# Optimization experiments

Hardware: AMD Instinct MI355X
Metric: run time of the kernel (lower is better)

## Reference

```python
import jax, jax.numpy as jnp
import numpy as np
from jax import lax

B, S, F, H, V, T = 64, 1024, 128, 512, 64, 64
SOS, EOS = 0, 1


def lstm_cell(x, h, c, W_ih, W_hh, b_ih, b_hh):
    # PyTorch LSTM gate order: i, f, g, o
    gates = x @ W_ih.T + h @ W_hh.T + b_ih + b_hh  # [B, 4H]
    i, f, g, o = jnp.split(gates, 4, axis=-1)
    c_new = jax.nn.sigmoid(f) * c + jax.nn.sigmoid(i) * jnp.tanh(g)
    h_new = jax.nn.sigmoid(o) * jnp.tanh(c_new)
    return h_new, c_new


def setup_inputs() -> dict:
    key = jax.random.key(0)
    ks = jax.random.split(key, 12)
    s = 0.05  # weight scale to avoid gate saturation
    return {
        "signal": jax.random.normal(ks[0], (B, S, F), jnp.float32),
        "target": jax.random.randint(ks[1], (B, T), 0, V),
        "enc_W_ih": jax.random.normal(ks[2], (4 * H, F), jnp.float32) * s,
        "enc_W_hh": jax.random.normal(ks[3], (4 * H, H), jnp.float32) * s,
        "enc_b_ih": jax.random.normal(ks[4], (4 * H,), jnp.float32) * s,
        "enc_b_hh": jax.random.normal(ks[5], (4 * H,), jnp.float32) * s,
        "dec_W_ih": jax.random.normal(ks[6], (4 * H, V), jnp.float32) * s,
        "dec_W_hh": jax.random.normal(ks[7], (4 * H, H), jnp.float32) * s,
        "dec_b_ih": jax.random.normal(ks[8], (4 * H,), jnp.float32) * s,
        "dec_b_hh": jax.random.normal(ks[9], (4 * H,), jnp.float32) * s,
        "out_W": jax.random.normal(ks[10], (V, H), jnp.float32) * s,
        "out_b": jax.random.normal(ks[11], (V,), jnp.float32) * s,
    }


def reference(signal, target, enc_W_ih, enc_W_hh, enc_b_ih, enc_b_hh,
              dec_W_ih, dec_W_hh, dec_b_ih, dec_b_hh, out_W, out_b):
    b = signal.shape[0]
    hdim = enc_W_hh.shape[1]
    vocab = out_b.shape[0]
    n_steps = target.shape[1]  # max_loop = target.size(1)

    # ---- encoder LSTM (only final hidden state is used downstream) ----
    def enc_step(carry, x_t):
        h, c = carry
        h, c = lstm_cell(x_t, h, c, enc_W_ih, enc_W_hh, enc_b_ih, enc_b_hh)
        return (h, c), None

    h0 = jnp.zeros((b, hdim), signal.dtype)
    (h, c), _ = lax.scan(enc_step, (h0, h0), jnp.swapaxes(signal, 0, 1))

    # ---- decoder: teacher-start (one-hot target[:,0]) then greedy feedback ----
    inp0 = jax.nn.one_hot(target[:, 0], vocab, dtype=signal.dtype)  # [B, V]

    def dec_step(carry, _):
        h, c, x = carry
        x = jax.nn.relu(x)  # F.relu on one-hot input (faithful to source)
        h, c = lstm_cell(x, h, c, dec_W_ih, dec_W_hh, dec_b_ih, dec_b_hh)
        logits = h @ out_W.T + out_b  # [B, V]
        nxt = jax.nn.one_hot(jnp.argmax(logits, axis=-1), vocab, dtype=x.dtype)
        return (h, c, nxt), logits

    (_, _, _), logits = lax.scan(dec_step, (h, c, inp0), None, length=n_steps)
    logits = jnp.swapaxes(logits, 0, 1)  # [B, T, V]
    return jax.nn.log_softmax(logits, axis=-1)
```

## Files before the change

kernel.cpp:

```cpp
#include <hip/hip_runtime.h>
#include <cstddef>
#include <math.h>

#define NGROUP 4
#define WPG    32
#define NWG    128
#define BPG    16
#define BB  64
#define HH  512
#define TT  64
#define VV  64
#define FF  128
#define SS  1024

typedef _Float16 f16;
typedef _Float16 f16x8 __attribute__((ext_vector_type(8)));
typedef float    f32x4 __attribute__((ext_vector_type(4)));
typedef unsigned int u32;
typedef u32 u32x4 __attribute__((ext_vector_type(4)));
typedef unsigned long long u64;

#define C1 4.8828125e-4f
#define C2 2.384185791015625e-7f

__device__ __forceinline__ void split8(const float* __restrict__ p, f16x8& hi, f16x8& lo) {
  f32x4 u = *(const f32x4*)p;
  f32x4 v = *(const f32x4*)(p + 4);
#pragma unroll
  for (int j = 0; j < 4; ++j) {
    f16 a = (f16)u[j]; hi[j]   = a; lo[j]   = (f16)((u[j] - (float)a) * 2048.0f);
    f16 b = (f16)v[j]; hi[4+j] = b; lo[4+j] = (f16)((v[j] - (float)b) * 2048.0f);
  }
}
__device__ __forceinline__ float sigmf_(float x) { return 1.0f / (1.0f + expf(-x)); }

__device__ __forceinline__ f32x4 ld16f(const void* p) {
  f32x4 r;
  asm volatile("global_load_dwordx4 %0, %1, off sc0 sc1" : "=v"(r) : "v"(p) : "memory");
  return r;
}
__device__ __forceinline__ void st4f(u32* p, u32 v) {
  __hip_atomic_store(p, v, __ATOMIC_RELAXED, __HIP_MEMORY_SCOPE_AGENT);
}
__device__ __forceinline__ void st4ff(float* p, float v) {
  __hip_atomic_store(p, v, __ATOMIC_RELAXED, __HIP_MEMORY_SCOPE_AGENT);
}
__device__ __forceinline__ u32 ld4f(const u32* p) {
  return __hip_atomic_load(p, __ATOMIC_RELAXED, __HIP_MEMORY_SCOPE_AGENT);
}
#define VMWAIT asm volatile("s_waitcnt vmcnt(0)" ::: "memory")

__device__ __forceinline__ void wait_flags(const u32* flags, u32 target, int lane) {
  const u32* a = flags + (size_t)(lane & 31) * 32;
  while (!__all(ld4f(a) >= target))
    __builtin_amdgcn_s_sleep(1);
}

#define MFMA(d, a, b) d = __builtin_amdgcn_mfma_f32_16x16x32_f16(a, b, d, 0, 0, 0)

#define STAGE_H(src_)                                                         \
  { const u32* src = (src_) + (size_t)(tid >> 4) * 256;                       \
    const int cq_ = tid & 15;                                                 \
    f32x4 sv[4];                                                              \
    _Pragma("unroll") for (int u2 = 0; u2 < 4; ++u2)                          \
      sv[u2] = ld16f(src + cq_*4 + u2*64);                                    \
    VMWAIT;                                                                   \
    _Pragma("unroll") for (int u2 = 0; u2 < 4; ++u2)                          \
      asm volatile("" : "+v"(sv[u2]));                                        \
    __builtin_amdgcn_sched_barrier(0);                                        \
    const int r_ = tid >> 4;                                                  \
    const size_t swz = (size_t)((r_ & 7) << 4);                               \
    _Pragma("unroll") for (int u2 = 0; u2 < 4; ++u2) {                        \
      size_t off = ((size_t)r_*1024 + (size_t)cq_*16 + (size_t)u2*256) ^ swz; \
      *(u32x4*)((char*)sh_h + off) = __builtin_bit_cast(u32x4, sv[u2]);       \
    } }                                                                       \
  __syncthreads();

#define LDA(s, ah)                                                            \
  { size_t o_ = ((size_t)mn * 1024 + (size_t)(s) * 64 + (size_t)(q8 * 2))     \
                ^ (size_t)((mn & 7) << 4);                                    \
    ah = *(const f16x8*)((const char*)sh_h + o_); }

#define HPART()                                                               \
  _Pragma("unroll") for (int s = 0; s < 16; ++s) {                            \
    f16x8 ah; LDA(s, ah);                                                     \
    MFMA(acc0, ah, whh_h[s]);                                                 \
    MFMA(acc1, ah, whh_l[s]);                                                 \
  }

#define XPART(ts)                                                             \
  { acc0 = zero4; acc1 = zero4; acc2 = zero4;                                 \
    const float* sb = sig + (size_t)(gb + mn) * (SS * FF) + (size_t)(ts) * FF;\
    _Pragma("unroll") for (int s = 0; s < 4; ++s) {                           \
      f16x8 xh, xl;                                                           \
      split8(sb + s * 32 + q8, xh, xl);                                       \
      MFMA(acc0, xh, wih_h[s]);                                               \
      MFMA(acc1, xl, wih_h[s]);                                               \
      MFMA(acc1, xh, wih_l[s]);                                               \
      MFMA(acc2, xl, wih_l[s]);                                               \
    } }

#define GWRITE()                                                              \
  _Pragma("unroll") for (int r = 0; r < 4; ++r)                               \
    gate_buf[w][q * 4 + r][mn] = acc0[r] + C1 * acc1[r] + C2 * acc2[r];

#define HSTORE(dst)                                                           \
  { f16 hh = (f16)h;                                                          \
    u32 mine = (u32)__builtin_bit_cast(unsigned short, hh);                   \
    u32 part = (u32)__shfl_xor((int)mine, 1, 64);                             \
    if ((tid & 1) == 0)                                                       \
      st4f((dst) + (size_t)cb * 256 + p * 8 + (ck >> 1), mine | (part << 16)); }

__global__ void __launch_bounds__(256, 1) lstm_seq2seq(
    const float* __restrict__ sig,
    const int*   __restrict__ tgt,
    const float* __restrict__ eWih,
    const float* __restrict__ eWhh,
    const float* __restrict__ eBih,
    const float* __restrict__ eBhh,
    const float* __restrict__ dWih,
    const float* __restrict__ dWhh,
    const float* __restrict__ dBih,
    const float* __restrict__ dBhh,
    const float* __restrict__ oW,
    const float* __restrict__ oB,
    float*       __restrict__ out,
    unsigned char* __restrict__ ws)
{
  const int wg = blockIdx.x;
  const int g  = wg >> 5;
  const int p  = wg & 31;
  const int gb = g * BPG;
  u32* fl     = (u32*)ws + (size_t)g * 1024;
  u32* idxbuf = (u32*)(ws + 16384);
  u32* h16[2] = { (u32*)(ws + 20480) + (size_t)(g*2 + 0) * 4096,
                  (u32*)(ws + 20480) + (size_t)(g*2 + 1) * 4096 };
  float* hfg  = (float*)(ws + 151552) + (size_t)g * 8192;

  const int tid  = threadIdx.x;
  const int w    = tid >> 6;
  const int lane = tid & 63;
  const int q    = lane >> 4;
  const int mn   = lane & 15;
  const int q8   = q * 8;
  const int row  = w * HH + p * 16 + mn;
  const int cb   = tid >> 4;
  const int ck   = tid & 15;
  const int crow = p * 16 + ck;

  __shared__ __attribute__((aligned(16))) f16 sh_h[16 * 512];
  __shared__ float gate_buf[4][16][17];
  __shared__ float bias_buf[4][16];
  __shared__ __attribute__((aligned(16))) float hrow[512];
  __shared__ double psum[64];

  f16x8 whh_h[16], whh_l[16], wih_h[4], wih_l[4];
#pragma unroll
  for (int s = 0; s < 16; ++s)
    split8(eWhh + (size_t)row * HH + s * 32 + q8, whh_h[s], whh_l[s]);
#pragma unroll
  for (int s = 0; s < 4; ++s)
    split8(eWih + (size_t)row * FF + s * 32 + q8, wih_h[s], wih_l[s]);
  if (tid < 64) {
    int g4 = tid >> 4, kl = tid & 15;
    int r = g4 * HH + p * 16 + kl;
    bias_buf[g4][kl] = eBih[r] + eBhh[r];
  }
  if (p == 0 && tid < BPG)
    st4f(idxbuf + gb + tid, (u32)tgt[(size_t)(gb + tid) * TT]);
  __syncthreads();

  float c_reg = 0.f;
  int cur = 0;
  const f32x4 zero4 = {0.f, 0.f, 0.f, 0.f};
  f32x4 acc0, acc1, acc2;

  XPART(0)
  for (int t = 0; t < SS; ++t) {
    wait_flags(fl, (u32)t, lane);
    STAGE_H(h16[cur])
    HPART()
    GWRITE()
    __syncthreads();
    {
      float gi = gate_buf[0][cb][ck] + bias_buf[0][ck];
      float gf = gate_buf[1][cb][ck] + bias_buf[1][ck];
      float gg = gate_buf[2][cb][ck] + bias_buf[2][ck];
      float go = gate_buf[3][cb][ck] + bias_buf[3][ck];
      float c  = sigmf_(gf) * c_reg + sigmf_(gi) * tanhf(gg);
      float h  = sigmf_(go) * tanhf(c);
      c_reg = c;
      HSTORE(h16[cur ^ 1])
    }
    XPART(t + 1 < SS ? t + 1 : SS - 1)
    VMWAIT;
    __syncthreads();
    if (tid == 0) st4f(fl + p * 32, (u32)(t + 1));
    cur ^= 1;
  }

#pragma unroll
  for (int s = 0; s < 16; ++s)
    split8(dWhh + (size_t)row * HH + s * 32 + q8, whh_h[s], whh_l[s]);
  __syncthreads();
  if (tid < 64) {
    int g4 = tid >> 4, kl = tid & 15;
    int r = g4 * HH + p * 16 + kl;
    bias_buf[g4][kl] = dBih[r] + dBhh[r];
  }
  __syncthreads();

  for (int t = 0; t < TT; ++t) {
    wait_flags(fl, (u32)(SS + 2 * t), lane);
    acc0 = zero4; acc1 = zero4; acc2 = zero4;
    STAGE_H(h16[cur])
    HPART()
    GWRITE()
    __syncthreads();
    {
      int ib = (int)ld4f(idxbuf + gb + cb);
      float gi = gate_buf[0][cb][ck] + bias_buf[0][ck] + dWih[(size_t)(0*HH + crow) * VV + ib];
      float gf = gate_buf[1][cb][ck] + bias_buf[1][ck] + dWih[(size_t)(1*HH + crow) * VV + ib];
      float gg = gate_buf[2][cb][ck] + bias_buf[2][ck] + dWih[(size_t)(2*HH + crow) * VV + ib];
      float go = gate_buf[3][cb][ck] + bias_buf[3][ck] + dWih[(size_t)(3*HH + crow) * VV + ib];
      float c  = sigmf_(gf) * c_reg + sigmf_(gi) * tanhf(gg);
      float h  = sigmf_(go) * tanhf(c);
      c_reg = c;
      HSTORE(h16[cur ^ 1])
      st4ff(hfg + (size_t)cb * HH + crow, h);
    }
    VMWAIT;
    __syncthreads();
    if (tid == 0) st4f(fl + p * 32, (u32)(SS + 2 * t + 1));
    int nxt = cur ^ 1;

    wait_flags(fl, (u32)(SS + 2 * t + 1), lane);
    if (p < BPG) {
      if (tid < 128) {
        f32x4 hv = ld16f(hfg + (size_t)p * HH + tid * 4);
        VMWAIT;
        *(f32x4*)&hrow[tid * 4] = hv;
      }
      __syncthreads();
      double acc = 0.0;
      if (w < 2) {
        const float* wr = oW + (size_t)lane * HH + w * 256;
        const float* hr = hrow + w * 256;
#pragma unroll 4
        for (int kc = 0; kc < 64; ++kc) {
          f32x4 hv = *(const f32x4*)(hr + kc * 4);
          f32x4 wv = *(const f32x4*)(wr + kc * 4);
          acc += (double)hv[0]*(double)wv[0] + (double)hv[1]*(double)wv[1]
               + (double)hv[2]*(double)wv[2] + (double)hv[3]*(double)wv[3];
        }
        if (w == 1) psum[lane] = acc;
      }
      __syncthreads();
      if (w == 0) {
        double l = acc + psum[lane] + (double)oB[lane];
        double mx = l; int ai = lane;
#pragma unroll
        for (int o = 32; o > 0; o >>= 1) {
          double om = __shfl_xor(mx, o, 64);
          int    oi = __shfl_xor(ai, o, 64);
          if (om > mx || (om == mx && oi < ai)) { mx = om; ai = oi; }
        }
        double se = exp(l - mx);
#pragma unroll
        for (int o = 32; o > 0; o >>= 1) se += __shfl_xor(se, o, 64);
        double lse = mx + log(se);
        out[((size_t)(gb + p) * TT + t) * VV + lane] = (float)(l - lse);
        if (lane == 0) st4f(idxbuf + gb + p, (u32)ai);
      }
    }
    VMWAIT;
    __syncthreads();
    if (tid == 0) st4f(fl + p * 32, (u32)(SS + 2 * t + 2));
    cur = nxt;
  }
}

extern "C" void kernel_launch(void* const* d_in, const int* in_sizes, int n_in,
                              void* d_out, int out_size, void* d_ws, size_t ws_size,
                              hipStream_t stream) {
  (void)in_sizes; (void)n_in; (void)out_size; (void)ws_size;
  hipMemsetAsync(d_ws, 0, 151552, stream);
  lstm_seq2seq<<<dim3(NWG), dim3(256), 0, stream>>>(
      (const float*)d_in[0],  (const int*)d_in[1],
      (const float*)d_in[2],  (const float*)d_in[3],
      (const float*)d_in[4],  (const float*)d_in[5],
      (const float*)d_in[6],  (const float*)d_in[7],
      (const float*)d_in[8],  (const float*)d_in[9],
      (const float*)d_in[10], (const float*)d_in[11],
      (float*)d_out, (unsigned char*)d_ws);
}
```

Measured before the change: 5.016 ms.

## Halve workgroups per batch group, giving each block two 16-row hidden slices

Cuts the persistent grid from 32 to 16 workgroups per batch group. Each workgroup now holds two 16-row weight slices in registers and issues twice the MFMAs per step, and each thread computes two hidden units, packing them into one store. This reduces the number of participants in the per-step cross-workgroup flag barrier and halves redundant h staging, at the cost of doubling per-block compute and register pressure on the serial critical path.

```diff
diff --git a/kernel.cpp b/kernel.cpp
--- a/kernel.cpp
+++ b/kernel.cpp
@@ -3,10 +3,9 @@
 #include <math.h>
 
 #define NGROUP 4
-#define WPG    32
-#define NWG    128
+#define WPG    16
+#define NWG    64
 #define BPG    16
-#define BB  64
 #define HH  512
 #define TT  64
 #define VV  64
@@ -17,6 +16,7 @@
 typedef _Float16 f16x8 __attribute__((ext_vector_type(8)));
 typedef float    f32x4 __attribute__((ext_vector_type(4)));
 typedef unsigned int u32;
+typedef unsigned short u16;
 typedef u32 u32x4 __attribute__((ext_vector_type(4)));
 typedef unsigned long long u64;
 
@@ -42,7 +42,7 @@
 __device__ __forceinline__ void st4f(u32* p, u32 v) {
   __hip_atomic_store(p, v, __ATOMIC_RELAXED, __HIP_MEMORY_SCOPE_AGENT);
 }
-__device__ __forceinline__ void st4ff(float* p, float v) {
+__device__ __forceinline__ void st8f(u64* p, u64 v) {
   __hip_atomic_store(p, v, __ATOMIC_RELAXED, __HIP_MEMORY_SCOPE_AGENT);
 }
 __device__ __forceinline__ u32 ld4f(const u32* p) {
@@ -51,7 +51,7 @@
 #define VMWAIT asm volatile("s_waitcnt vmcnt(0)" ::: "memory")
 
 __device__ __forceinline__ void wait_flags(const u32* flags, u32 target, int lane) {
-  const u32* a = flags + (size_t)(lane & 31) * 32;
+  const u32* a = flags + (size_t)(lane & 15) * 32;
   while (!__all(ld4f(a) >= target))
     __builtin_amdgcn_s_sleep(1);
 }
@@ -84,32 +84,29 @@
 #define HPART()                                                               \
   _Pragma("unroll") for (int s = 0; s < 16; ++s) {                            \
     f16x8 ah; LDA(s, ah);                                                     \
-    MFMA(acc0, ah, whh_h[s]);                                                 \
-    MFMA(acc1, ah, whh_l[s]);                                                 \
-  }
+    _Pragma("unroll") for (int j = 0; j < 2; ++j) {                           \
+      MFMA(acc0[j], ah, whh_h[j][s]);                                         \
+      MFMA(acc1[j], ah, whh_l[j][s]);                                         \
+    } }
 
 #define XPART(ts)                                                             \
-  { acc0 = zero4; acc1 = zero4; acc2 = zero4;                                 \
+  { _Pragma("unroll") for (int j = 0; j < 2; ++j) {                           \
+      acc0[j] = zero4; acc1[j] = zero4; acc2[j] = zero4; }                    \
     const float* sb = sig + (size_t)(gb + mn) * (SS * FF) + (size_t)(ts) * FF;\
     _Pragma("unroll") for (int s = 0; s < 4; ++s) {                           \
       f16x8 xh, xl;                                                           \
       split8(sb + s * 32 + q8, xh, xl);                                       \
-      MFMA(acc0, xh, wih_h[s]);                                               \
-      MFMA(acc1, xl, wih_h[s]);                                               \
-      MFMA(acc1, xh, wih_l[s]);                                               \
-      MFMA(acc2, xl, wih_l[s]);                                               \
-    } }
+      _Pragma("unroll") for (int j = 0; j < 2; ++j) {                         \
+        MFMA(acc0[j], xh, wih_h[j][s]);                                       \
+        MFMA(acc1[j], xl, wih_h[j][s]);                                       \
+        MFMA(acc1[j], xh, wih_l[j][s]);                                       \
+        MFMA(acc2[j], xl, wih_l[j][s]);                                       \
+      } } }
 
 #define GWRITE()                                                              \
-  _Pragma("unroll") for (int r = 0; r < 4; ++r)                               \
-    gate_buf[w][q * 4 + r][mn] = acc0[r] + C1 * acc1[r] + C2 * acc2[r];
-
-#define HSTORE(dst)                                                           \
-  { f16 hh = (f16)h;                                                          \
-    u32 mine = (u32)__builtin_bit_cast(unsigned short, hh);                   \
-    u32 part = (u32)__shfl_xor((int)mine, 1, 64);                             \
-    if ((tid & 1) == 0)                                                       \
-      st4f((dst) + (size_t)cb * 256 + p * 8 + (ck >> 1), mine | (part << 16)); }
+  _Pragma("unroll") for (int j = 0; j < 2; ++j)                               \
+    _Pragma("unroll") for (int r = 0; r < 4; ++r)                             \
+      gate_buf[w][q*4 + r][j*16 + mn] = acc0[j][r] + C1*acc1[j][r] + C2*acc2[j][r];
 
 __global__ void __launch_bounds__(256, 1) lstm_seq2seq(
     const float* __restrict__ sig,
@@ -128,8 +125,8 @@
     unsigned char* __restrict__ ws)
 {
   const int wg = blockIdx.x;
-  const int g  = wg >> 5;
-  const int p  = wg & 31;
+  const int g  = wg >> 4;
+  const int p  = wg & 15;
   const int gb = g * BPG;
   u32* fl     = (u32*)ws + (size_t)g * 1024;
   u32* idxbuf = (u32*)(ws + 16384);
@@ -143,37 +140,43 @@
   const int q    = lane >> 4;
   const int mn   = lane & 15;
   const int q8   = q * 8;
-  const int row  = w * HH + p * 16 + mn;
+  const int row0 = w * HH + p * 32 + mn;
+  const int row1 = row0 + 16;
   const int cb   = tid >> 4;
   const int ck   = tid & 15;
-  const int crow = p * 16 + ck;
+  const int crow0 = p * 32 + 2 * ck;
+  const int crow1 = crow0 + 1;
 
   __shared__ __attribute__((aligned(16))) f16 sh_h[16 * 512];
-  __shared__ float gate_buf[4][16][17];
-  __shared__ float bias_buf[4][16];
+  __shared__ float gate_buf[4][16][35];
+  __shared__ float bias_buf[4][32];
   __shared__ __attribute__((aligned(16))) float hrow[512];
   __shared__ double psum[64];
 
-  f16x8 whh_h[16], whh_l[16], wih_h[4], wih_l[4];
-#pragma unroll
-  for (int s = 0; s < 16; ++s)
-    split8(eWhh + (size_t)row * HH + s * 32 + q8, whh_h[s], whh_l[s]);
-#pragma unroll
-  for (int s = 0; s < 4; ++s)
-    split8(eWih + (size_t)row * FF + s * 32 + q8, wih_h[s], wih_l[s]);
-  if (tid < 64) {
-    int g4 = tid >> 4, kl = tid & 15;
-    int r = g4 * HH + p * 16 + kl;
+  f16x8 whh_h[2][16], whh_l[2][16], wih_h[2][4], wih_l[2][4];
+#pragma unroll
+  for (int s = 0; s < 16; ++s) {
+    split8(eWhh + (size_t)row0 * HH + s * 32 + q8, whh_h[0][s], whh_l[0][s]);
+    split8(eWhh + (size_t)row1 * HH + s * 32 + q8, whh_h[1][s], whh_l[1][s]);
+  }
+#pragma unroll
+  for (int s = 0; s < 4; ++s) {
+    split8(eWih + (size_t)row0 * FF + s * 32 + q8, wih_h[0][s], wih_l[0][s]);
+    split8(eWih + (size_t)row1 * FF + s * 32 + q8, wih_h[1][s], wih_l[1][s]);
+  }
+  if (tid < 128) {
+    int g4 = tid >> 5, kl = tid & 31;
+    int r = g4 * HH + p * 32 + kl;
     bias_buf[g4][kl] = eBih[r] + eBhh[r];
   }
   if (p == 0 && tid < BPG)
     st4f(idxbuf + gb + tid, (u32)tgt[(size_t)(gb + tid) * TT]);
   __syncthreads();
 
-  float c_reg = 0.f;
+  float c_reg0 = 0.f, c_reg1 = 0.f;
   int cur = 0;
   const f32x4 zero4 = {0.f, 0.f, 0.f, 0.f};
-  f32x4 acc0, acc1, acc2;
+  f32x4 acc0[2], acc1[2], acc2[2];
 
   XPART(0)
   for (int t = 0; t < SS; ++t) {
@@ -183,14 +186,22 @@
     GWRITE()
     __syncthreads();
     {
-      float gi = gate_buf[0][cb][ck] + bias_buf[0][ck];
-      float gf = gate_buf[1][cb][ck] + bias_buf[1][ck];
-      float gg = gate_buf[2][cb][ck] + bias_buf[2][ck];
-      float go = gate_buf[3][cb][ck] + bias_buf[3][ck];
-      float c  = sigmf_(gf) * c_reg + sigmf_(gi) * tanhf(gg);
-      float h  = sigmf_(go) * tanhf(c);
-      c_reg = c;
-      HSTORE(h16[cur ^ 1])
+      float gi0 = gate_buf[0][cb][2*ck]   + bias_buf[0][2*ck];
+      float gf0 = gate_buf[1][cb][2*ck]   + bias_buf[1][2*ck];
+      float gg0 = gate_buf[2][cb][2*ck]   + bias_buf[2][2*ck];
+      float go0 = gate_buf[3][cb][2*ck]   + bias_buf[3][2*ck];
+      float gi1 = gate_buf[0][cb][2*ck+1] + bias_buf[0][2*ck+1];
+      float gf1 = gate_buf[1][cb][2*ck+1] + bias_buf[1][2*ck+1];
+      float gg1 = gate_buf[2][cb][2*ck+1] + bias_buf[2][2*ck+1];
+      float go1 = gate_buf[3][cb][2*ck+1] + bias_buf[3][2*ck+1];
+      float c0 = sigmf_(gf0) * c_reg0 + sigmf_(gi0) * tanhf(gg0);
+      float c1 = sigmf_(gf1) * c_reg1 + sigmf_(gi1) * tanhf(gg1);
+      float h0 = sigmf_(go0) * tanhf(c0);
+      float h1 = sigmf_(go1) * tanhf(c1);
+      c_reg0 = c0; c_reg1 = c1;
+      u32 pk = (u32)__builtin_bit_cast(u16, (f16)h0)
+             | ((u32)__builtin_bit_cast(u16, (f16)h1) << 16);
+      st4f(h16[cur ^ 1] + (size_t)cb * 256 + p * 16 + ck, pk);
     }
     XPART(t + 1 < SS ? t + 1 : SS - 1)
     VMWAIT;
@@ -200,34 +211,47 @@
   }
 
 #pragma unroll
-  for (int s = 0; s < 16; ++s)
-    split8(dWhh + (size_t)row * HH + s * 32 + q8, whh_h[s], whh_l[s]);
+  for (int s = 0; s < 16; ++s) {
+    split8(dWhh + (size_t)row0 * HH + s * 32 + q8, whh_h[0][s], whh_l[0][s]);
+    split8(dWhh + (size_t)row1 * HH + s * 32 + q8, whh_h[1][s], whh_l[1][s]);
+  }
   __syncthreads();
-  if (tid < 64) {
-    int g4 = tid >> 4, kl = tid & 15;
-    int r = g4 * HH + p * 16 + kl;
+  if (tid < 128) {
+    int g4 = tid >> 5, kl = tid & 31;
+    int r = g4 * HH + p * 32 + kl;
     bias_buf[g4][kl] = dBih[r] + dBhh[r];
   }
   __syncthreads();
 
   for (int t = 0; t < TT; ++t) {
     wait_flags(fl, (u32)(SS + 2 * t), lane);
-    acc0 = zero4; acc1 = zero4; acc2 = zero4;
+#pragma unroll
+    for (int j = 0; j < 2; ++j) { acc0[j] = zero4; acc1[j] = zero4; acc2[j] = zero4; }
     STAGE_H(h16[cur])
     HPART()
     GWRITE()
     __syncthreads();
     {
       int ib = (int)ld4f(idxbuf + gb + cb);
-      float gi = gate_buf[0][cb][ck] + bias_buf[0][ck] + dWih[(size_t)(0*HH + crow) * VV + ib];
-      float gf = gate_buf[1][cb][ck] + bias_buf[1][ck] + dWih[(size_t)(1*HH + crow) * VV + ib];
-      float gg = gate_buf[2][cb][ck] + bias_buf[2][ck] + dWih[(size_t)(2*HH + crow) * VV + ib];
-      float go = gate_buf[3][cb][ck] + bias_buf[3][ck] + dWih[(size_t)(3*HH + crow) * VV + ib];
-      float c  = sigmf_(gf) * c_reg + sigmf_(gi) * tanhf(gg);
-      float h  = sigmf_(go) * tanhf(c);
-      c_reg = c;
-      HSTORE(h16[cur ^ 1])
-      st4ff(hfg + (size_t)cb * HH + crow, h);
+      float gi0 = gate_buf[0][cb][2*ck]   + bias_buf[0][2*ck]   + dWih[(size_t)(0*HH + crow0) * VV + ib];
+      float gf0 = gate_buf[1][cb][2*ck]   + bias_buf[1][2*ck]   + dWih[(size_t)(1*HH + crow0) * VV + ib];
+      float gg0 = gate_buf[2][cb][2*ck]   + bias_buf[2][2*ck]   + dWih[(size_t)(2*HH + crow0) * VV + ib];
+      float go0 = gate_buf[3][cb][2*ck]   + bias_buf[3][2*ck]   + dWih[(size_t)(3*HH + crow0) * VV + ib];
+      float gi1 = gate_buf[0][cb][2*ck+1] + bias_buf[0][2*ck+1] + dWih[(size_t)(0*HH + crow1) * VV + ib];
+      float gf1 = gate_buf[1][cb][2*ck+1] + bias_buf[1][2*ck+1] + dWih[(size_t)(1*HH + crow1) * VV + ib];
+      float gg1 = gate_buf[2][cb][2*ck+1] + bias_buf[2][2*ck+1] + dWih[(size_t)(2*HH + crow1) * VV + ib];
+      float go1 = gate_buf[3][cb][2*ck+1] + bias_buf[3][2*ck+1] + dWih[(size_t)(3*HH + crow1) * VV + ib];
+      float c0 = sigmf_(gf0) * c_reg0 + sigmf_(gi0) * tanhf(gg0);
+      float c1 = sigmf_(gf1) * c_reg1 + sigmf_(gi1) * tanhf(gg1);
+      float h0 = sigmf_(go0) * tanhf(c0);
+      float h1 = sigmf_(go1) * tanhf(c1);
+      c_reg0 = c0; c_reg1 = c1;
+      u32 pk = (u32)__builtin_bit_cast(u16, (f16)h0)
+             | ((u32)__builtin_bit_cast(u16, (f16)h1) << 16);
+      st4f(h16[cur ^ 1] + (size_t)cb * 256 + p * 16 + ck, pk);
+      u64 pf = (u64)__builtin_bit_cast(u32, h0)
+             | ((u64)__builtin_bit_cast(u32, h1) << 32);
+      st8f((u64*)(hfg + (size_t)cb * HH + crow0), pf);
     }
     VMWAIT;
     __syncthreads();
```

After: 6.108 ms. +21.8%, slower.

## Split each batch group into two interleaved half-batches to overlap barrier latency

Applied to the files above, without the earlier changes.

Each 32-workgroup group now handles two independent 8-row half-batches (A and B) in alternation. While one half waits on the cross-workgroup flag barrier, the other half's staging, MFMA and gate work proceeds, and flag release is moved to right after staging. The aim is to hide inter-workgroup synchronisation latency on the serial recurrence. In exchange, half of each 16-row MFMA tile is wasted, barrier count per step doubles, and the flag protocol becomes more complex.

```diff
diff --git a/kernel.cpp b/kernel.cpp
--- a/kernel.cpp
+++ b/kernel.cpp
@@ -2,11 +2,8 @@
 #include <cstddef>
 #include <math.h>
 
-#define NGROUP 4
-#define WPG    32
-#define NWG    128
-#define BPG    16
-#define BB  64
+#define NWG 128
+#define BPG 8
 #define HH  512
 #define TT  64
 #define VV  64
@@ -17,6 +14,7 @@
 typedef _Float16 f16x8 __attribute__((ext_vector_type(8)));
 typedef float    f32x4 __attribute__((ext_vector_type(4)));
 typedef unsigned int u32;
+typedef unsigned short u16;
 typedef u32 u32x4 __attribute__((ext_vector_type(4)));
 typedef unsigned long long u64;
 
@@ -58,55 +56,50 @@
 
 #define MFMA(d, a, b) d = __builtin_amdgcn_mfma_f32_16x16x32_f16(a, b, d, 0, 0, 0)
 
-#define STAGE_H(src_)                                                         \
-  { const u32* src = (src_) + (size_t)(tid >> 4) * 256;                       \
-    const int cq_ = tid & 15;                                                 \
-    f32x4 sv[4];                                                              \
-    _Pragma("unroll") for (int u2 = 0; u2 < 4; ++u2)                          \
-      sv[u2] = ld16f(src + cq_*4 + u2*64);                                    \
+#define STAGE_H2(src_, SH)                                                    \
+  { const u32* src = (src_) + (size_t)(tid >> 5) * 256 + (size_t)(tid & 31) * 8; \
+    f32x4 sv0 = ld16f(src), sv1 = ld16f(src + 4);                             \
     VMWAIT;                                                                   \
-    _Pragma("unroll") for (int u2 = 0; u2 < 4; ++u2)                          \
-      asm volatile("" : "+v"(sv[u2]));                                        \
+    asm volatile("" : "+v"(sv0), "+v"(sv1));                                  \
     __builtin_amdgcn_sched_barrier(0);                                        \
-    const int r_ = tid >> 4;                                                  \
-    const size_t swz = (size_t)((r_ & 7) << 4);                               \
-    _Pragma("unroll") for (int u2 = 0; u2 < 4; ++u2) {                        \
-      size_t off = ((size_t)r_*1024 + (size_t)cq_*16 + (size_t)u2*256) ^ swz; \
-      *(u32x4*)((char*)sh_h + off) = __builtin_bit_cast(u32x4, sv[u2]);       \
-    } }                                                                       \
-  __syncthreads();
-
-#define LDA(s, ah)                                                            \
-  { size_t o_ = ((size_t)mn * 1024 + (size_t)(s) * 64 + (size_t)(q8 * 2))     \
-                ^ (size_t)((mn & 7) << 4);                                    \
-    ah = *(const f16x8*)((const char*)sh_h + o_); }
-
-#define HPART()                                                               \
+    const int r_ = tid >> 5;                                                  \
+    const size_t base_ = (size_t)r_ * 1024 + (size_t)(tid & 31) * 32;         \
+    const size_t swz_ = (size_t)(r_ << 4);                                    \
+    *(u32x4*)((char*)(SH) + (base_ ^ swz_))        = __builtin_bit_cast(u32x4, sv0); \
+    *(u32x4*)((char*)(SH) + ((base_ + 16) ^ swz_)) = __builtin_bit_cast(u32x4, sv1); \
+  }
+
+#define LDA2(SH, s, ah)                                                       \
+  { size_t o_ = ((size_t)rmn * 1024 + (size_t)(s) * 64 + (size_t)(q8 * 2))    \
+                ^ (size_t)(rmn << 4);                                         \
+    ah = *(const f16x8*)((const char*)(SH) + o_); }
+
+#define HPART2(SH, A0, A1)                                                    \
   _Pragma("unroll") for (int s = 0; s < 16; ++s) {                            \
-    f16x8 ah; LDA(s, ah);                                                     \
-    MFMA(acc0, ah, whh_h[s]);                                                 \
-    MFMA(acc1, ah, whh_l[s]);                                                 \
-  }
-
-#define XPART(ts)                                                             \
-  { acc0 = zero4; acc1 = zero4; acc2 = zero4;                                 \
-    const float* sb = sig + (size_t)(gb + mn) * (SS * FF) + (size_t)(ts) * FF;\
+    f16x8 ah; LDA2(SH, s, ah);                                                \
+    MFMA(A0, ah, whh_h[s]);                                                   \
+    MFMA(A1, ah, whh_l[s]);                                                   \
+  }
+
+#define XPART2(gbX, ts, A0, A1, A2)                                           \
+  { A0 = zero4; A1 = zero4; A2 = zero4;                                       \
+    const float* sb = sig + (size_t)((gbX) + rmn) * (SS * FF) + (size_t)(ts) * FF; \
     _Pragma("unroll") for (int s = 0; s < 4; ++s) {                           \
       f16x8 xh, xl;                                                           \
       split8(sb + s * 32 + q8, xh, xl);                                       \
-      MFMA(acc0, xh, wih_h[s]);                                               \
-      MFMA(acc1, xl, wih_h[s]);                                               \
-      MFMA(acc1, xh, wih_l[s]);                                               \
-      MFMA(acc2, xl, wih_l[s]);                                               \
+      MFMA(A0, xh, wih_h[s]);                                                 \
+      MFMA(A1, xl, wih_h[s]);                                                 \
+      MFMA(A1, xh, wih_l[s]);                                                 \
+      MFMA(A2, xl, wih_l[s]);                                                 \
     } }
 
-#define GWRITE()                                                              \
-  _Pragma("unroll") for (int r = 0; r < 4; ++r)                               \
-    gate_buf[w][q * 4 + r][mn] = acc0[r] + C1 * acc1[r] + C2 * acc2[r];
-
-#define HSTORE(dst)                                                           \
-  { f16 hh = (f16)h;                                                          \
-    u32 mine = (u32)__builtin_bit_cast(unsigned short, hh);                   \
+#define GWRITE2(A0, A1, A2)                                                   \
+  if (q < 2)                                                                  \
+    _Pragma("unroll") for (int r = 0; r < 4; ++r)                             \
+      gate_buf[w][q * 4 + r][mn] = A0[r] + C1 * A1[r] + C2 * A2[r];
+
+#define HSTORE2(dst, h)                                                       \
+  { u32 mine = (u32)__builtin_bit_cast(u16, (f16)(h));                        \
     u32 part = (u32)__shfl_xor((int)mine, 1, 64);                             \
     if ((tid & 1) == 0)                                                       \
       st4f((dst) + (size_t)cb * 256 + p * 8 + (ck >> 1), mine | (part << 16)); }
@@ -127,29 +120,35 @@
     float*       __restrict__ out,
     unsigned char* __restrict__ ws)
 {
-  const int wg = blockIdx.x;
-  const int g  = wg >> 5;
-  const int p  = wg & 31;
-  const int gb = g * BPG;
-  u32* fl     = (u32*)ws + (size_t)g * 1024;
+  const int wg   = blockIdx.x;
+  const int pair = wg >> 5;
+  const int p    = wg & 31;
+  const int gA   = 2 * pair, gB = 2 * pair + 1;
+  const int gbA  = gA * BPG, gbB = gB * BPG;
+  u32* fl     = (u32*)ws + (size_t)pair * 1024;
   u32* idxbuf = (u32*)(ws + 16384);
-  u32* h16[2] = { (u32*)(ws + 20480) + (size_t)(g*2 + 0) * 4096,
-                  (u32*)(ws + 20480) + (size_t)(g*2 + 1) * 4096 };
-  float* hfg  = (float*)(ws + 151552) + (size_t)g * 8192;
+  u32* h16A[2] = { (u32*)(ws + 20480) + (size_t)(gA*2 + 0) * 2048,
+                   (u32*)(ws + 20480) + (size_t)(gA*2 + 1) * 2048 };
+  u32* h16B[2] = { (u32*)(ws + 20480) + (size_t)(gB*2 + 0) * 2048,
+                   (u32*)(ws + 20480) + (size_t)(gB*2 + 1) * 2048 };
+  float* hfgA = (float*)(ws + 151552) + (size_t)gA * 4096;
+  float* hfgB = (float*)(ws + 151552) + (size_t)gB * 4096;
 
   const int tid  = threadIdx.x;
   const int w    = tid >> 6;
   const int lane = tid & 63;
   const int q    = lane >> 4;
   const int mn   = lane & 15;
+  const int rmn  = mn & 7;
   const int q8   = q * 8;
   const int row  = w * HH + p * 16 + mn;
   const int cb   = tid >> 4;
   const int ck   = tid & 15;
   const int crow = p * 16 + ck;
 
-  __shared__ __attribute__((aligned(16))) f16 sh_h[16 * 512];
-  __shared__ float gate_buf[4][16][17];
+  __shared__ __attribute__((aligned(16))) f16 sh_A[8 * 512];
+  __shared__ __attribute__((aligned(16))) f16 sh_B[8 * 512];
+  __shared__ float gate_buf[4][8][17];
   __shared__ float bias_buf[4][16];
   __shared__ __attribute__((aligned(16))) float hrow[512];
   __shared__ double psum[64];
@@ -166,37 +165,53 @@
     int r = g4 * HH + p * 16 + kl;
     bias_buf[g4][kl] = eBih[r] + eBhh[r];
   }
-  if (p == 0 && tid < BPG)
-    st4f(idxbuf + gb + tid, (u32)tgt[(size_t)(gb + tid) * TT]);
+  if (p == 0 && tid < 16)
+    st4f(idxbuf + pair * 16 + tid, (u32)tgt[(size_t)(pair * 16 + tid) * TT]);
   __syncthreads();
 
-  float c_reg = 0.f;
-  int cur = 0;
+  float c_regA = 0.f, c_regB = 0.f;
   const f32x4 zero4 = {0.f, 0.f, 0.f, 0.f};
-  f32x4 acc0, acc1, acc2;
-
-  XPART(0)
+  f32x4 accA0, accA1, accA2, accB0, accB1, accB2;
+
+  XPART2(gbA, 0, accA0, accA1, accA2)
   for (int t = 0; t < SS; ++t) {
-    wait_flags(fl, (u32)t, lane);
-    STAGE_H(h16[cur])
-    HPART()
-    GWRITE()
-    __syncthreads();
-    {
+    const int pb = t & 1;
+    if (t) wait_flags(fl, (u32)(2*t - 1), lane);
+    STAGE_H2(h16A[pb], sh_A)
+    if (t && tid == 0) st4f(fl + p * 32, (u32)(2*t));
+    __syncthreads();
+    HPART2(sh_A, accA0, accA1)
+    GWRITE2(accA0, accA1, accA2)
+    __syncthreads();
+    if (tid < 128) {
       float gi = gate_buf[0][cb][ck] + bias_buf[0][ck];
       float gf = gate_buf[1][cb][ck] + bias_buf[1][ck];
       float gg = gate_buf[2][cb][ck] + bias_buf[2][ck];
       float go = gate_buf[3][cb][ck] + bias_buf[3][ck];
-      float c  = sigmf_(gf) * c_reg + sigmf_(gi) * tanhf(gg);
+      float c  = sigmf_(gf) * c_regA + sigmf_(gi) * tanhf(gg);
       float h  = sigmf_(go) * tanhf(c);
-      c_reg = c;
-      HSTORE(h16[cur ^ 1])
-    }
-    XPART(t + 1 < SS ? t + 1 : SS - 1)
-    VMWAIT;
-    __syncthreads();
-    if (tid == 0) st4f(fl + p * 32, (u32)(t + 1));
-    cur ^= 1;
+      c_regA = c;
+      HSTORE2(h16A[pb ^ 1], h)
+    }
+    XPART2(gbB, t, accB0, accB1, accB2)
+    wait_flags(fl, (u32)(2*t), lane);
+    STAGE_H2(h16B[pb], sh_B)
+    if (tid == 0) st4f(fl + p * 32, (u32)(2*t + 1));
+    __syncthreads();
+    HPART2(sh_B, accB0, accB1)
+    GWRITE2(accB0, accB1, accB2)
+    __syncthreads();
+    if (tid < 128) {
+      float gi = gate_buf[0][cb][ck] + bias_buf[0][ck];
+      float gf = gate_buf[1][cb][ck] + bias_buf[1][ck];
+      float gg = gate_buf[2][cb][ck] + bias_buf[2][ck];
+      float go = gate_buf[3][cb][ck] + bias_buf[3][ck];
+      float c  = sigmf_(gf) * c_regB + sigmf_(gi) * tanhf(gg);
+      float h  = sigmf_(go) * tanhf(c);
+      c_regB = c;
+      HSTORE2(h16B[pb ^ 1], h)
+    }
+    XPART2(gbA, t + 1 < SS ? t + 1 : SS - 1, accA0, accA1, accA2)
   }
 
 #pragma unroll
@@ -211,33 +226,56 @@
   __syncthreads();
 
   for (int t = 0; t < TT; ++t) {
-    wait_flags(fl, (u32)(SS + 2 * t), lane);
-    acc0 = zero4; acc1 = zero4; acc2 = zero4;
-    STAGE_H(h16[cur])
-    HPART()
-    GWRITE()
-    __syncthreads();
-    {
-      int ib = (int)ld4f(idxbuf + gb + cb);
+    const int pb = (SS + t) & 1;
+    const u32 base = (u32)(2 * SS + 4 * t);
+    wait_flags(fl, t ? base : (u32)(2 * SS - 1), lane);
+    STAGE_H2(h16A[pb], sh_A)
+    if (tid == 0) st4f(fl + p * 32, base + 1);
+    __syncthreads();
+    accA0 = zero4; accA1 = zero4; accA2 = zero4;
+    HPART2(sh_A, accA0, accA1)
+    GWRITE2(accA0, accA1, accA2)
+    __syncthreads();
+    if (tid < 128) {
+      int ib = (int)ld4f(idxbuf + gbA + cb);
       float gi = gate_buf[0][cb][ck] + bias_buf[0][ck] + dWih[(size_t)(0*HH + crow) * VV + ib];
       float gf = gate_buf[1][cb][ck] + bias_buf[1][ck] + dWih[(size_t)(1*HH + crow) * VV + ib];
       float gg = gate_buf[2][cb][ck] + bias_buf[2][ck] + dWih[(size_t)(2*HH + crow) * VV + ib];
       float go = gate_buf[3][cb][ck] + bias_buf[3][ck] + dWih[(size_t)(3*HH + crow) * VV + ib];
-      float c  = sigmf_(gf) * c_reg + sigmf_(gi) * tanhf(gg);
+      float c  = sigmf_(gf) * c_regA + sigmf_(gi) * tanhf(gg);
       float h  = sigmf_(go) * tanhf(c);
-      c_reg = c;
-      HSTORE(h16[cur ^ 1])
-      st4ff(hfg + (size_t)cb * HH + crow, h);
+      c_regA = c;
+      HSTORE2(h16A[pb ^ 1], h)
+      st4ff(hfgA + (size_t)cb * HH + crow, h);
+    }
+    wait_flags(fl, base + 1, lane);
+    STAGE_H2(h16B[pb], sh_B)
+    if (tid == 0) st4f(fl + p * 32, base + 2);
+    __syncthreads();
+    accB0 = zero4; accB1 = zero4; accB2 = zero4;
+    HPART2(sh_B, accB0, accB1)
+    GWRITE2(accB0, accB1, accB2)
+    __syncthreads();
+    if (tid < 128) {
+      int ib = (int)ld4f(idxbuf + gbB + cb);
+      float gi = gate_buf[0][cb][ck] + bias_buf[0][ck] + dWih[(size_t)(0*HH + crow) * VV + ib];
+      float gf = gate_buf[1][cb][ck] + bias_buf[1][ck] + dWih[(size_t)(1*HH + crow) * VV + ib];
+      float gg = gate_buf[2][cb][ck] + bias_buf[2][ck] + dWih[(size_t)(2*HH + crow) * VV + ib];
+      float go = gate_buf[3][cb][ck] + bias_buf[3][ck] + dWih[(size_t)(3*HH + crow) * VV + ib];
+      float c  = sigmf_(gf) * c_regB + sigmf_(gi) * tanhf(gg);
+      float h  = sigmf_(go) * tanhf(c);
+      c_regB = c;
+      HSTORE2(h16B[pb ^ 1], h)
+      st4ff(hfgB + (size_t)cb * HH + crow, h);
     }
     VMWAIT;
     __syncthreads();
-    if (tid == 0) st4f(fl + p * 32, (u32)(SS + 2 * t + 1));
-    int nxt = cur ^ 1;
-
-    wait_flags(fl, (u32)(SS + 2 * t + 1), lane);
-    if (p < BPG) {
+    if (tid == 0) st4f(fl + p * 32, base + 3);
+    wait_flags(fl, base + 3, lane);
+    if (p < 16) {
+      const float* hsrc = ((p >> 3) ? hfgB : hfgA) + (size_t)(p & 7) * HH;
       if (tid < 128) {
-        f32x4 hv = ld16f(hfg + (size_t)p * HH + tid * 4);
+        f32x4 hv = ld16f(hsrc + (size_t)tid * 4);
         VMWAIT;
         *(f32x4*)&hrow[tid * 4] = hv;
       }
@@ -269,14 +307,13 @@
 #pragma unroll
         for (int o = 32; o > 0; o >>= 1) se += __shfl_xor(se, o, 64);
         double lse = mx + log(se);
-        out[((size_t)(gb + p) * TT + t) * VV + lane] = (float)(l - lse);
-        if (lane == 0) st4f(idxbuf + gb + p, (u32)ai);
+        out[((size_t)(pair * 16 + p) * TT + t) * VV + lane] = (float)(l - lse);
+        if (lane == 0) st4f(idxbuf + pair * 16 + p, (u32)ai);
       }
     }
     VMWAIT;
     __syncthreads();
-    if (tid == 0) st4f(fl + p * 32, (u32)(SS + 2 * t + 2));
-    cur = nxt;
+    if (tid == 0) st4f(fl + p * 32, base + 4);
   }
 }
 
```

After: 6.798 ms. +35.5%, slower.
